# Optimization experiments

Measured on AMD Instinct MI355X. Metric: run time of the kernel, lower is better.

## Reference

```python
import jax, jax.numpy as jnp
import numpy as np

B, DEC, ENC, HID, UNITS = 4, 256, 1024, 512, 128


def setup_inputs() -> dict:
    key = jax.random.key(0)
    k1, k2, k3, k4, k5, k6 = jax.random.split(key, 6)
    query = jax.random.normal(k1, (B, DEC, HID), dtype=jnp.float32)
    value = jax.random.normal(k2, (B, ENC, HID), dtype=jnp.float32)
    mask = jax.random.bernoulli(k3, 0.9, (B, ENC))  # bool, True = keep
    # Dense(units, use_bias=False) kernels, glorot-ish scaling
    W1 = jax.random.normal(k4, (HID, UNITS), dtype=jnp.float32) * (1.0 / np.sqrt(HID))
    W2 = jax.random.normal(k5, (HID, UNITS), dtype=jnp.float32) * (1.0 / np.sqrt(HID))
    # AdditiveAttention use_scale=True: learned per-unit scale vector
    scale = jax.random.normal(k6, (UNITS,), dtype=jnp.float32) * (1.0 / np.sqrt(UNITS))
    return {"query": query, "value": value, "mask": mask, "W1": W1, "W2": W2, "scale": scale}


def reference(query, value, mask, W1, W2, scale):
    # query: (B, DEC, HID), value: (B, ENC, HID), mask: (B, ENC) bool
    q = jnp.einsum("bqh,hu->bqu", query, W1)   # (B, DEC, U)
    k = jnp.einsum("beh,hu->beu", value, W2)   # (B, ENC, U)
    # Bahdanau additive score: sum_u scale_u * tanh(q + k)  -> (B, DEC, ENC)
    scores = jnp.einsum("bqeu,u->bqe", jnp.tanh(q[:, :, None, :] + k[:, None, :, :]), scale)
    neg = jnp.asarray(-1e9, scores.dtype)
    scores = jnp.where(mask[:, None, :], scores, neg)
    attention_weights = jax.nn.softmax(scores, axis=-1)   # (B, DEC, ENC)
    context_vector = jnp.einsum("bqe,beh->bqh", attention_weights, value)  # (B, DEC, HID)
    # query_mask is all-ones in the original module -> no-op on output
    return (context_vector, attention_weights)
```

## Files before the change

### kernel.cpp

```cpp
#include <hip/hip_runtime.h>
#include <cstddef>

#define B     4
#define DEC   256
#define ENC   1024
#define HID   512
#define UNITS 128

#define PROJ_SCALE 2.8853900817779268f

__global__ __launch_bounds__(256) void proj_kernel(
    const float* __restrict__ query, const float* __restrict__ value,
    const float* __restrict__ W1,    const float* __restrict__ W2,
    float* __restrict__ qbuf,        float* __restrict__ kbufT)
{
    __shared__ float part[4][8][UNITS];

    const int tid  = threadIdx.x;
    const int lane = tid & 63;
    const int wv   = __builtin_amdgcn_readfirstlane(tid >> 6);
    const int row0g = blockIdx.x * 8;
    const bool isQ = row0g < B * DEC;
    const float* X = isQ ? query : value;
    const float* W = isQ ? W1 : W2;
    const int row0 = isQ ? row0g : row0g - B * DEC;
    const int h0   = wv * 128;

    float acc0[8], acc1[8];
    #pragma unroll
    for (int r = 0; r < 8; ++r) { acc0[r] = 0.f; acc1[r] = 0.f; }

    const float* Xb = X + (size_t)row0 * HID + h0;
    const float* Wb = W + (size_t)h0 * UNITS;

    for (int h = 0; h < 128; h += 4) {
        const float wa0 = Wb[(h+0)*UNITS + lane], wb0 = Wb[(h+0)*UNITS + 64 + lane];
        const float wa1 = Wb[(h+1)*UNITS + lane], wb1 = Wb[(h+1)*UNITS + 64 + lane];
        const float wa2 = Wb[(h+2)*UNITS + lane], wb2 = Wb[(h+2)*UNITS + 64 + lane];
        const float wa3 = Wb[(h+3)*UNITS + lane], wb3 = Wb[(h+3)*UNITS + 64 + lane];
        #pragma unroll
        for (int r = 0; r < 8; ++r) {
            const float4 xv = *(const float4*)(Xb + r * HID + h);
            acc0[r] += xv.x*wa0 + xv.y*wa1 + xv.z*wa2 + xv.w*wa3;
            acc1[r] += xv.x*wb0 + xv.y*wb1 + xv.z*wb2 + xv.w*wb3;
        }
    }

    #pragma unroll
    for (int r = 0; r < 8; ++r) {
        part[wv][r][lane]      = acc0[r];
        part[wv][r][64 + lane] = acc1[r];
    }
    __syncthreads();

    #pragma unroll
    for (int k = 0; k < 4; ++k) {
        const int idx = tid + k * 256;
        const int r = idx >> 7, u = idx & (UNITS - 1);
        const float s = PROJ_SCALE *
            ((part[0][r][u] + part[1][r][u]) + (part[2][r][u] + part[3][r][u]));
        const int row = row0 + r;
        if (isQ) {
            qbuf[(size_t)row * UNITS + u] = s;
        } else {
            const int bb = row >> 10, e = row & (ENC - 1);
            const int c = u >> 2, j = u & 3;
            kbufT[((size_t)bb * 32 * ENC + (size_t)c * ENC + e) * 4 + j] = s;
        }
    }
}

__device__ __forceinline__ float sig_r(float a) {
    return __builtin_amdgcn_rcpf(1.f + __builtin_amdgcn_exp2f(a));
}

__global__ __launch_bounds__(512) void score_kernel(
    const float* __restrict__ qbuf, const float* __restrict__ kbufT,
    const int* __restrict__ mask,   const float* __restrict__ scale,
    float* __restrict__ attn_out)
{
    const int bi  = blockIdx.x;
    const int b   = (bi >> 1) & 3;
    const int dq0 = (((bi >> 3) << 1) | (bi & 1)) * 2;
    const int tid = threadIdx.x;

    float S0 = 0.f;
    for (int j = 0; j < UNITS; j += 4) {
        const float4 sv = *(const float4*)(scale + j);
        S0 += (sv.x + sv.y) + (sv.z + sv.w);
    }

    const float* q0 = qbuf + (size_t)(b * DEC + dq0) * UNITS;
    const float* q1 = q0 + UNITS;
    const float* kb = kbufT + (size_t)b * 32 * ENC * 4;

    float t0[2] = {0.f,0.f}, t1[2] = {0.f,0.f};
    for (int i = 0; i < 32; ++i) {
        const float4 qa = *(const float4*)(q0 + i * 4);
        const float4 qb = *(const float4*)(q1 + i * 4);
        const float4 sv = *(const float4*)(scale + i * 4);
        const float* kc = kb + (size_t)i * ENC * 4;
        #pragma unroll
        for (int ei = 0; ei < 2; ++ei) {
            const int e = tid + ei * 512;
            const float4 kv = *(const float4*)(kc + (size_t)e * 4);
            t0[ei] += sv.x * sig_r(qa.x + kv.x);
            t0[ei] += sv.y * sig_r(qa.y + kv.y);
            t0[ei] += sv.z * sig_r(qa.z + kv.z);
            t0[ei] += sv.w * sig_r(qa.w + kv.w);
            t1[ei] += sv.x * sig_r(qb.x + kv.x);
            t1[ei] += sv.y * sig_r(qb.y + kv.y);
            t1[ei] += sv.z * sig_r(qb.z + kv.z);
            t1[ei] += sv.w * sig_r(qb.w + kv.w);
        }
    }

    float s0[2], s1[2];
    #pragma unroll
    for (int ei = 0; ei < 2; ++ei) {
        const int m = mask[b * ENC + tid + ei * 512];
        s0[ei] = m ? (S0 - 2.f * t0[ei]) : -1e9f;
        s1[ei] = m ? (S0 - 2.f * t1[ei]) : -1e9f;
    }

    __shared__ float redm[2][8];
    __shared__ float reds[2][8];
    const int lane = tid & 63, wv = tid >> 6;

    float lm0 = fmaxf(s0[0], s0[1]);
    float lm1 = fmaxf(s1[0], s1[1]);
    #pragma unroll
    for (int off = 32; off > 0; off >>= 1) {
        lm0 = fmaxf(lm0, __shfl_down(lm0, off, 64));
        lm1 = fmaxf(lm1, __shfl_down(lm1, off, 64));
    }
    if (lane == 0) { redm[0][wv] = lm0; redm[1][wv] = lm1; }
    __syncthreads();
    float gm0 = redm[0][0], gm1 = redm[1][0];
    #pragma unroll
    for (int w = 1; w < 8; ++w) {
        gm0 = fmaxf(gm0, redm[0][w]);
        gm1 = fmaxf(gm1, redm[1][w]);
    }

    float w0[2], w1[2];
    float ls0 = 0.f, ls1 = 0.f;
    #pragma unroll
    for (int ei = 0; ei < 2; ++ei) {
        w0[ei] = __expf(s0[ei] - gm0); ls0 += w0[ei];
        w1[ei] = __expf(s1[ei] - gm1); ls1 += w1[ei];
    }
    #pragma unroll
    for (int off = 32; off > 0; off >>= 1) {
        ls0 += __shfl_down(ls0, off, 64);
        ls1 += __shfl_down(ls1, off, 64);
    }
    if (lane == 0) { reds[0][wv] = ls0; reds[1][wv] = ls1; }
    __syncthreads();
    float gs0 = 0.f, gs1 = 0.f;
    #pragma unroll
    for (int w = 0; w < 8; ++w) { gs0 += reds[0][w]; gs1 += reds[1][w]; }
    const float inv0 = __builtin_amdgcn_rcpf(gs0);
    const float inv1 = __builtin_amdgcn_rcpf(gs1);

    float* a0 = attn_out + (size_t)(b * DEC + dq0) * ENC;
    float* a1 = a0 + ENC;
    #pragma unroll
    for (int ei = 0; ei < 2; ++ei) {
        const int e = tid + ei * 512;
        a0[e] = w0[ei] * inv0;
        a1[e] = w1[ei] * inv1;
    }
}

__global__ __launch_bounds__(512) void ctx_kernel(
    const float* __restrict__ attn, const float* __restrict__ value,
    float* __restrict__ ctx)
{
    __shared__ float part[8][8][128];

    const int bi   = blockIdx.x;
    const int b    = (bi >> 1) & 3;
    const int idx  = ((bi >> 3) << 1) | (bi & 1);
    const int row0 = (idx >> 2) * 8;
    const int h0   = (idx & 3) * 128;
    const int tid  = threadIdx.x;
    const int lane = tid & 63;
    const int wv   = __builtin_amdgcn_readfirstlane(tid >> 6);

    float acc[8][2];
    #pragma unroll
    for (int r = 0; r < 8; ++r) { acc[r][0] = 0.f; acc[r][1] = 0.f; }

    const float* vb = value + (size_t)b * ENC * HID + h0 + lane * 2;
    const float* ab = attn + (size_t)(b * DEC + row0) * ENC;

    #pragma unroll
    for (int ec = 0; ec < 2; ++ec) {
        const int e0 = wv * 128 + ec * 64;
        float sc[8];
        #pragma unroll
        for (int r = 0; r < 8; ++r)
            sc[r] = ab[(size_t)r * ENC + e0 + lane];
        const float* vp = vb + (size_t)e0 * HID;
        #pragma unroll
        for (int l = 0; l < 64; ++l) {
            const float2 v2 = *(const float2*)(vp + (size_t)l * HID);
            #pragma unroll
            for (int r = 0; r < 8; ++r) {
                const float w = __builtin_bit_cast(float,
                    __builtin_amdgcn_readlane(__builtin_bit_cast(int, sc[r]), l));
                acc[r][0] += w * v2.x;
                acc[r][1] += w * v2.y;
            }
        }
    }

    #pragma unroll
    for (int r = 0; r < 8; ++r)
        *(float2*)&part[wv][r][lane * 2] = make_float2(acc[r][0], acc[r][1]);
    __syncthreads();

    #pragma unroll
    for (int k = 0; k < 2; ++k) {
        const int idx2 = tid + k * 512;
        const int r = idx2 >> 7, hh = idx2 & 127;
        float s = 0.f;
        #pragma unroll
        for (int w = 0; w < 8; ++w) s += part[w][r][hh];
        ctx[(size_t)(b * DEC + row0 + r) * HID + h0 + hh] = s;
    }
}

extern "C" void kernel_launch(void* const* d_in, const int* in_sizes, int n_in,
                              void* d_out, int out_size, void* d_ws, size_t ws_size,
                              hipStream_t stream) {
    const float* query = (const float*)d_in[0];
    const float* value = (const float*)d_in[1];
    const int*   mask  = (const int*)  d_in[2];
    const float* W1    = (const float*)d_in[3];
    const float* W2    = (const float*)d_in[4];
    const float* scale = (const float*)d_in[5];

    float* qbuf  = (float*)d_ws;
    float* kbufT = qbuf + (size_t)B * DEC * UNITS;

    float* ctx_out  = (float*)d_out;
    float* attn_out = ctx_out + (size_t)B * DEC * HID;

    proj_kernel <<<640, 256, 0, stream>>>(query, value, W1, W2, qbuf, kbufT);
    score_kernel<<<512, 512, 0, stream>>>(qbuf, kbufT, mask, scale, attn_out);
    ctx_kernel  <<<512, 512, 0, stream>>>(attn_out, value, ctx_out);
}
```

Before: 150.0 us.

## Widen score kernel to 1024 threads and stage attention rows in LDS for ctx

The score kernel now launches 1024 threads per block, so each thread handles a single encoder position rather than two. That doubles the wave count, and the block reductions now span 16 waves. The ctx kernel first copies the block's 8 attention rows into shared memory and reads them back as float4 broadcasts, replacing the per-lane readlane broadcasts from registers. The goal is more latency hiding in the transcendental-heavy score loop and fewer scalar readlane instructions in ctx. The cost is larger blocks that may limit occupancy and 32KB of extra LDS per ctx block.

```diff
diff --git a/kernel.cpp b/kernel.cpp
--- a/kernel.cpp
+++ b/kernel.cpp
@@ -74,7 +74,7 @@
     return __builtin_amdgcn_rcpf(1.f + __builtin_amdgcn_exp2f(a));
 }
 
-__global__ __launch_bounds__(512) void score_kernel(
+__global__ __launch_bounds__(1024) void score_kernel(
     const float* __restrict__ qbuf, const float* __restrict__ kbufT,
     const int* __restrict__ mask,   const float* __restrict__ scale,
     float* __restrict__ attn_out)
@@ -92,43 +92,33 @@
 
     const float* q0 = qbuf + (size_t)(b * DEC + dq0) * UNITS;
     const float* q1 = q0 + UNITS;
-    const float* kb = kbufT + (size_t)b * 32 * ENC * 4;
-
-    float t0[2] = {0.f,0.f}, t1[2] = {0.f,0.f};
+    const float* kc = kbufT + (size_t)b * 32 * ENC * 4 + (size_t)tid * 4;
+
+    float t0 = 0.f, t1 = 0.f;
     for (int i = 0; i < 32; ++i) {
         const float4 qa = *(const float4*)(q0 + i * 4);
         const float4 qb = *(const float4*)(q1 + i * 4);
         const float4 sv = *(const float4*)(scale + i * 4);
-        const float* kc = kb + (size_t)i * ENC * 4;
-        #pragma unroll
-        for (int ei = 0; ei < 2; ++ei) {
-            const int e = tid + ei * 512;
-            const float4 kv = *(const float4*)(kc + (size_t)e * 4);
-            t0[ei] += sv.x * sig_r(qa.x + kv.x);
-            t0[ei] += sv.y * sig_r(qa.y + kv.y);
-            t0[ei] += sv.z * sig_r(qa.z + kv.z);
-            t0[ei] += sv.w * sig_r(qa.w + kv.w);
-            t1[ei] += sv.x * sig_r(qb.x + kv.x);
-            t1[ei] += sv.y * sig_r(qb.y + kv.y);
-            t1[ei] += sv.z * sig_r(qb.z + kv.z);
-            t1[ei] += sv.w * sig_r(qb.w + kv.w);
-        }
-    }
-
-    float s0[2], s1[2];
-    #pragma unroll
-    for (int ei = 0; ei < 2; ++ei) {
-        const int m = mask[b * ENC + tid + ei * 512];
-        s0[ei] = m ? (S0 - 2.f * t0[ei]) : -1e9f;
-        s1[ei] = m ? (S0 - 2.f * t1[ei]) : -1e9f;
-    }
-
-    __shared__ float redm[2][8];
-    __shared__ float reds[2][8];
+        const float4 kv = *(const float4*)(kc + (size_t)i * ENC * 4);
+        t0 += sv.x * sig_r(qa.x + kv.x);
+        t0 += sv.y * sig_r(qa.y + kv.y);
+        t0 += sv.z * sig_r(qa.z + kv.z);
+        t0 += sv.w * sig_r(qa.w + kv.w);
+        t1 += sv.x * sig_r(qb.x + kv.x);
+        t1 += sv.y * sig_r(qb.y + kv.y);
+        t1 += sv.z * sig_r(qb.z + kv.z);
+        t1 += sv.w * sig_r(qb.w + kv.w);
+    }
+
+    const int m = mask[b * ENC + tid];
+    const float s0 = m ? (S0 - 2.f * t0) : -1e9f;
+    const float s1 = m ? (S0 - 2.f * t1) : -1e9f;
+
+    __shared__ float redm[2][16];
+    __shared__ float reds[2][16];
     const int lane = tid & 63, wv = tid >> 6;
 
-    float lm0 = fmaxf(s0[0], s0[1]);
-    float lm1 = fmaxf(s1[0], s1[1]);
+    float lm0 = s0, lm1 = s1;
     #pragma unroll
     for (int off = 32; off > 0; off >>= 1) {
         lm0 = fmaxf(lm0, __shfl_down(lm0, off, 64));
@@ -138,18 +128,14 @@
     __syncthreads();
     float gm0 = redm[0][0], gm1 = redm[1][0];
     #pragma unroll
-    for (int w = 1; w < 8; ++w) {
+    for (int w = 1; w < 16; ++w) {
         gm0 = fmaxf(gm0, redm[0][w]);
         gm1 = fmaxf(gm1, redm[1][w]);
     }
 
-    float w0[2], w1[2];
-    float ls0 = 0.f, ls1 = 0.f;
-    #pragma unroll
-    for (int ei = 0; ei < 2; ++ei) {
-        w0[ei] = __expf(s0[ei] - gm0); ls0 += w0[ei];
-        w1[ei] = __expf(s1[ei] - gm1); ls1 += w1[ei];
-    }
+    const float w0 = __expf(s0 - gm0);
+    const float w1 = __expf(s1 - gm1);
+    float ls0 = w0, ls1 = w1;
     #pragma unroll
     for (int off = 32; off > 0; off >>= 1) {
         ls0 += __shfl_down(ls0, off, 64);
@@ -159,24 +145,21 @@
     __syncthreads();
     float gs0 = 0.f, gs1 = 0.f;
     #pragma unroll
-    for (int w = 0; w < 8; ++w) { gs0 += reds[0][w]; gs1 += reds[1][w]; }
+    for (int w = 0; w < 16; ++w) { gs0 += reds[0][w]; gs1 += reds[1][w]; }
     const float inv0 = __builtin_amdgcn_rcpf(gs0);
     const float inv1 = __builtin_amdgcn_rcpf(gs1);
 
     float* a0 = attn_out + (size_t)(b * DEC + dq0) * ENC;
-    float* a1 = a0 + ENC;
-    #pragma unroll
-    for (int ei = 0; ei < 2; ++ei) {
-        const int e = tid + ei * 512;
-        a0[e] = w0[ei] * inv0;
-        a1[e] = w1[ei] * inv1;
-    }
+    attn_out[(size_t)(b * DEC + dq0) * ENC + tid]       = w0 * inv0;
+    attn_out[(size_t)(b * DEC + dq0 + 1) * ENC + tid]   = w1 * inv1;
+    (void)a0;
 }
 
 __global__ __launch_bounds__(512) void ctx_kernel(
     const float* __restrict__ attn, const float* __restrict__ value,
     float* __restrict__ ctx)
 {
+    __shared__ float attnS[8][ENC];
     __shared__ float part[8][8][128];
 
     const int bi   = blockIdx.x;
@@ -188,31 +171,39 @@
     const int lane = tid & 63;
     const int wv   = __builtin_amdgcn_readfirstlane(tid >> 6);
 
+    const float* ab = attn + (size_t)(b * DEC + row0) * ENC;
+    #pragma unroll
+    for (int r = 0; r < 8; ++r) {
+        const float2 v = *(const float2*)(ab + (size_t)r * ENC + tid * 2);
+        *(float2*)&attnS[r][tid * 2] = v;
+    }
+    __syncthreads();
+
     float acc[8][2];
     #pragma unroll
     for (int r = 0; r < 8; ++r) { acc[r][0] = 0.f; acc[r][1] = 0.f; }
 
     const float* vb = value + (size_t)b * ENC * HID + h0 + lane * 2;
-    const float* ab = attn + (size_t)(b * DEC + row0) * ENC;
-
-    #pragma unroll
-    for (int ec = 0; ec < 2; ++ec) {
-        const int e0 = wv * 128 + ec * 64;
-        float sc[8];
+    const int e0 = wv * 128;
+
+    for (int g = 0; g < 32; ++g) {
+        const int eg = e0 + g * 4;
+        float4 w4[8];
         #pragma unroll
         for (int r = 0; r < 8; ++r)
-            sc[r] = ab[(size_t)r * ENC + e0 + lane];
-        const float* vp = vb + (size_t)e0 * HID;
-        #pragma unroll
-        for (int l = 0; l < 64; ++l) {
-            const float2 v2 = *(const float2*)(vp + (size_t)l * HID);
+            w4[r] = *(const float4*)&attnS[r][eg];
+        const float* vp = vb + (size_t)eg * HID;
+        #pragma unroll
+        for (int j = 0; j < 4; ++j) {
+            const float2 v2 = *(const float2*)(vp + (size_t)j * HID);
+            const float* wj = (const float*)&w4[0] + j;
             #pragma unroll
             for (int r = 0; r < 8; ++r) {
-                const float w = __builtin_bit_cast(float,
-                    __builtin_amdgcn_readlane(__builtin_bit_cast(int, sc[r]), l));
+                const float w = ((const float*)&w4[r])[j];
                 acc[r][0] += w * v2.x;
                 acc[r][1] += w * v2.y;
             }
+            (void)wj;
         }
     }
 
@@ -248,7 +239,7 @@
     float* ctx_out  = (float*)d_out;
     float* attn_out = ctx_out + (size_t)B * DEC * HID;
 
-    proj_kernel <<<640, 256, 0, stream>>>(query, value, W1, W2, qbuf, kbufT);
-    score_kernel<<<512, 512, 0, stream>>>(qbuf, kbufT, mask, scale, attn_out);
-    ctx_kernel  <<<512, 512, 0, stream>>>(attn_out, value, ctx_out);
-}
+    proj_kernel <<<640,  256, 0, stream>>>(query, value, W1, W2, qbuf, kbufT);
+    score_kernel<<<512, 1024, 0, stream>>>(qbuf, kbufT, mask, scale, attn_out);
+    ctx_kernel  <<<512,  512, 0, stream>>>(attn_out, value, ctx_out);
+}
```

Measured after the change: 149.5 us. No clear change (-0.3%).
